# Performance work log

Measured on AMD Instinct MI355X. Metric: run time of the kernel, lower is better.

Reference implementation:

```python
import jax, jax.numpy as jnp
import numpy as np

VOCAB = 32000
DIM = 512
FFN = 4 * DIM
LAYERS_PER_BLOCK = [2, 2, 2]
THRESHOLDS = [3.5e-05, 4.0e-05, 1.0]
N_LAYERS = sum(LAYERS_PER_BLOCK)
B, S = 4, 1024


def setup_inputs() -> dict:
    key = jax.random.key(0)
    ks = jax.random.split(key, 8)
    x = jax.random.randint(ks[0], (B, S), 0, VOCAB)
    emb = jax.random.normal(ks[1], (VOCAB, DIM), jnp.float32) * 0.02
    head = jax.random.normal(ks[2], (VOCAB, DIM), jnp.float32) * (1.0 / np.sqrt(DIM))
    Wv = jax.random.normal(ks[3], (N_LAYERS, DIM, DIM), jnp.float32) * 0.02
    Wo = jax.random.normal(ks[4], (N_LAYERS, DIM, DIM), jnp.float32) * 0.02
    W1 = jax.random.normal(ks[5], (N_LAYERS, DIM, FFN), jnp.float32) * 0.02
    W2 = jax.random.normal(ks[6], (N_LAYERS, FFN, DIM), jnp.float32) * 0.02
    ln1_s = jnp.ones((N_LAYERS, DIM), jnp.float32)
    ln1_b = jnp.zeros((N_LAYERS, DIM), jnp.float32)
    ln2_s = jnp.ones((N_LAYERS, DIM), jnp.float32)
    ln2_b = jnp.zeros((N_LAYERS, DIM), jnp.float32)
    return {"x": x, "emb": emb, "head": head, "Wv": Wv, "Wo": Wo,
            "W1": W1, "W2": W2, "ln1_s": ln1_s, "ln1_b": ln1_b,
            "ln2_s": ln2_s, "ln2_b": ln2_b}


def _ln(x, s, b):
    m = jnp.mean(x, axis=-1, keepdims=True)
    v = jnp.mean((x - m) ** 2, axis=-1, keepdims=True)
    return (x - m) * jax.lax.rsqrt(v + 1e-5) * s + b


def reference(x, emb, head, Wv, Wo, W1, W2, ln1_s, ln1_b, ln2_s, ln2_b):
    T = B * S
    h = emb[x.reshape(-1)]                      # (T, dim) embedding gather
    active = jnp.ones((T,), dtype=bool)
    final_logits = jnp.zeros((T, VOCAB), jnp.float32)
    layer = 0
    n_blocks = len(LAYERS_PER_BLOCK)
    for b_idx, (n_l, thr) in enumerate(zip(LAYERS_PER_BLOCK, THRESHOLDS)):
        hb = h
        for l in range(layer, layer + n_l):
            # seq_len==1 attention: softmax over single key == 1 -> out = V @ Wo
            hn = _ln(hb, ln1_s[l], ln1_b[l])
            hb = hb + (hn @ Wv[l]) @ Wo[l]
            hn2 = _ln(hb, ln2_s[l], ln2_b[l])
            hb = hb + jax.nn.gelu(hn2 @ W1[l]) @ W2[l]
        layer += n_l
        logits = hb @ head.T                    # (T, vocab)
        conf = jnp.max(jax.nn.softmax(logits, axis=-1), axis=-1)
        is_last = b_idx == n_blocks - 1
        should_exit = conf > thr
        exit_now = active & (should_exit | is_last)   # scatter exiting tokens
        final_logits = jnp.where(exit_now[:, None], logits, final_logits)
        cont = active & ~exit_now
        h = jnp.where(cont[:, None], hb, h)           # only continuing tokens updated
        active = cont
    return final_logits.reshape(B, S, VOCAB)
```

## Files before the change

### kernel.cpp

```cpp
#include <hip/hip_runtime.h>
#include <hip/hip_bf16.h>
#include <math.h>

#define TT 4096
#define DIM 512
#define FFN 2048
#define NVOCAB 32000

typedef __attribute__((ext_vector_type(8))) short short8_t;
typedef __attribute__((ext_vector_type(4))) float f32x4;

__device__ __forceinline__ float gelu_f(float x) {
    float x3 = x * x * x;
    float u = 0.7978845608028654f * (x + 0.044715f * x3);
    return 0.5f * x * (1.0f + tanhf(u));
}

__device__ __forceinline__ unsigned short f2bf_rn(float f) {
    unsigned u = __float_as_uint(f);
    u += 0x7FFFu + ((u >> 16) & 1u);
    return (unsigned short)(u >> 16);
}

__global__ __launch_bounds__(128) void gather_kernel(const int* __restrict__ x,
                                                     const float* __restrict__ emb,
                                                     float* __restrict__ h,
                                                     int* __restrict__ flags) {
    int t = blockIdx.x;
    int idx = x[t];
    const float4 v = *(const float4*)&emb[(size_t)idx * DIM + threadIdx.x * 4];
    *(float4*)&h[(size_t)t * DIM + threadIdx.x * 4] = v;
    if (threadIdx.x == 0) flags[t] = 1;
}

__global__ __launch_bounds__(256) void cvt_hilo(const float* __restrict__ src,
                                                short* __restrict__ hi,
                                                short* __restrict__ lo, int n4) {
    int i = blockIdx.x * 256 + threadIdx.x;
    if (i >= n4) return;
    float4 v = *(const float4*)&src[(size_t)i * 4];
    float f[4] = {v.x, v.y, v.z, v.w};
    short4 hv, lv;
    short* hp = &hv.x;
    short* lp = &lv.x;
#pragma unroll
    for (int j = 0; j < 4; ++j) {
        unsigned short hb = f2bf_rn(f[j]);
        float hf = __uint_as_float((unsigned)hb << 16);
        unsigned short lb = f2bf_rn(f[j] - hf);
        hp[j] = (short)hb;
        lp[j] = (short)lb;
    }
    *(short4*)&hi[(size_t)i * 4] = hv;
    *(short4*)&lo[(size_t)i * 4] = lv;
}

__global__ __launch_bounds__(256) void cvt_bf16(const float* __restrict__ src,
                                                short* __restrict__ hi, int n4) {
    int i = blockIdx.x * 256 + threadIdx.x;
    if (i >= n4) return;
    float4 v = *(const float4*)&src[(size_t)i * 4];
    float f[4] = {v.x, v.y, v.z, v.w};
    short4 hv;
    short* hp = &hv.x;
#pragma unroll
    for (int j = 0; j < 4; ++j) hp[j] = (short)f2bf_rn(f[j]);
    *(short4*)&hi[(size_t)i * 4] = hv;
}

__global__ __launch_bounds__(256) void cvt_w_t(const float* __restrict__ W,
                                               short* __restrict__ hiT,
                                               short* __restrict__ loT,
                                               int K, int N) {
    __shared__ short hs[32][36];
    __shared__ short ls[32][36];
    const int n0 = blockIdx.x * 32, k0 = blockIdx.y * 32;
    const int r = threadIdx.x >> 3, c4 = (threadIdx.x & 7) << 2;
    float4 v = *(const float4*)&W[(size_t)(k0 + r) * N + n0 + c4];
    float f[4] = {v.x, v.y, v.z, v.w};
#pragma unroll
    for (int j = 0; j < 4; ++j) {
        unsigned short hb = f2bf_rn(f[j]);
        float hf = __uint_as_float((unsigned)hb << 16);
        unsigned short lb = f2bf_rn(f[j] - hf);
        hs[r][c4 + j] = (short)hb;
        ls[r][c4 + j] = (short)lb;
    }
    __syncthreads();
    const int nr = threadIdx.x >> 3, kc4 = (threadIdx.x & 7) << 2;
    short4 hv, lv;
    short* hp = &hv.x;
    short* lp = &lv.x;
#pragma unroll
    for (int j = 0; j < 4; ++j) {
        hp[j] = hs[kc4 + j][nr];
        lp[j] = ls[kc4 + j][nr];
    }
    *(short4*)&hiT[(size_t)(n0 + nr) * K + k0 + kc4] = hv;
    *(short4*)&loT[(size_t)(n0 + nr) * K + k0 + kc4] = lv;
}

template<bool IDX>
__global__ __launch_bounds__(256) void ln_kernel(const float* __restrict__ x,
                                                 const float* __restrict__ gam,
                                                 const float* __restrict__ bet,
                                                 float* __restrict__ out,
                                                 const int* __restrict__ idx,
                                                 const int* __restrict__ cnt) {
    int wv = threadIdx.x >> 6, lane = threadIdx.x & 63;
    int p = (blockIdx.x << 2) | wv;
    if (IDX && p >= *cnt) return;
    int t = IDX ? idx[p] : p;
    const float* row = x + (size_t)t * DIM;
    int base = lane * 8;
    float4 v0 = *(const float4*)&row[base];
    float4 v1 = *(const float4*)&row[base + 4];
    float s = v0.x + v0.y + v0.z + v0.w + v1.x + v1.y + v1.z + v1.w;
#pragma unroll
    for (int o = 32; o; o >>= 1) s += __shfl_xor(s, o, 64);
    float mean = s * (1.0f / (float)DIM);
    float d0 = v0.x - mean, d1 = v0.y - mean, d2 = v0.z - mean, d3 = v0.w - mean;
    float d4 = v1.x - mean, d5 = v1.y - mean, d6 = v1.z - mean, d7 = v1.w - mean;
    float q = d0*d0 + d1*d1 + d2*d2 + d3*d3 + d4*d4 + d5*d5 + d6*d6 + d7*d7;
#pragma unroll
    for (int o = 32; o; o >>= 1) q += __shfl_xor(q, o, 64);
    float var = q * (1.0f / (float)DIM);
    float rs = 1.0f / sqrtf(var + 1e-5f);
    float4 g0 = *(const float4*)&gam[base];
    float4 g1 = *(const float4*)&gam[base + 4];
    float4 b0 = *(const float4*)&bet[base];
    float4 b1 = *(const float4*)&bet[base + 4];
    float4 o0, o1;
    o0.x = d0 * rs * g0.x + b0.x;  o0.y = d1 * rs * g0.y + b0.y;
    o0.z = d2 * rs * g0.z + b0.z;  o0.w = d3 * rs * g0.w + b0.w;
    o1.x = d4 * rs * g1.x + b1.x;  o1.y = d5 * rs * g1.y + b1.y;
    o1.z = d6 * rs * g1.z + b1.z;  o1.w = d7 * rs * g1.w + b1.w;
    float* orow = out + (size_t)p * DIM;
    *(float4*)&orow[base] = o0;
    *(float4*)&orow[base + 4] = o1;
}

__global__ __launch_bounds__(256) void ln_hilo(const float* __restrict__ x,
                                               const float* __restrict__ gam,
                                               const float* __restrict__ bet,
                                               short* __restrict__ ohi,
                                               short* __restrict__ olo) {
    int wv = threadIdx.x >> 6, lane = threadIdx.x & 63;
    int t = (blockIdx.x << 2) | wv;
    const float* row = x + (size_t)t * DIM;
    int base = lane * 8;
    float4 v0 = *(const float4*)&row[base];
    float4 v1 = *(const float4*)&row[base + 4];
    float s = v0.x + v0.y + v0.z + v0.w + v1.x + v1.y + v1.z + v1.w;
#pragma unroll
    for (int o = 32; o; o >>= 1) s += __shfl_xor(s, o, 64);
    float mean = s * (1.0f / (float)DIM);
    float d[8] = {v0.x - mean, v0.y - mean, v0.z - mean, v0.w - mean,
                  v1.x - mean, v1.y - mean, v1.z - mean, v1.w - mean};
    float q = 0.0f;
#pragma unroll
    for (int j = 0; j < 8; ++j) q += d[j] * d[j];
#pragma unroll
    for (int o = 32; o; o >>= 1) q += __shfl_xor(q, o, 64);
    float var = q * (1.0f / (float)DIM);
    float rs = 1.0f / sqrtf(var + 1e-5f);
    float g[8], bb[8];
    *(float4*)&g[0] = *(const float4*)&gam[base];
    *(float4*)&g[4] = *(const float4*)&gam[base + 4];
    *(float4*)&bb[0] = *(const float4*)&bet[base];
    *(float4*)&bb[4] = *(const float4*)&bet[base + 4];
    short8_t hv, lv;
#pragma unroll
    for (int j = 0; j < 8; ++j) {
        float val = d[j] * rs * g[j] + bb[j];
        unsigned short hb = f2bf_rn(val);
        float hf = __uint_as_float((unsigned)hb << 16);
        hv[j] = (short)hb;
        lv[j] = (short)f2bf_rn(val - hf);
    }
    *(short8_t*)&ohi[(size_t)t * DIM + base] = hv;
    *(short8_t*)&olo[(size_t)t * DIM + base] = lv;
}

template<int EPI>
__global__ __launch_bounds__(256) void gemm_l_mfma(const short* __restrict__ Ah,
                                                   const short* __restrict__ Al,
                                                   const short* __restrict__ Bh,
                                                   const short* __restrict__ Bl,
                                                   float* __restrict__ Cf,
                                                   short* __restrict__ oHi,
                                                   short* __restrict__ oLo,
                                                   int N, int K) {
    __shared__ __align__(16) short sm[16384];
    short* sAh = sm;
    short* sAl = sm + 4096;
    short* sBh = sm + 8192;
    short* sBl = sm + 12288;
    const int tid = threadIdx.x;
    const int wv = tid >> 6, lane = tid & 63;
    const int m0 = blockIdx.x * 128;
    const int n0 = blockIdx.y * 128;
    const int wm = (wv & 1) * 64, wn = (wv >> 1) * 64;
    const int r16 = lane >> 2;
    const int gsw = ((lane & 3) ^ (r16 & 3)) << 3;
    const int fr = lane & 15;
    const int q = lane >> 4;

    f32x4 acc[4][4];
#pragma unroll
    for (int i = 0; i < 4; ++i)
#pragma unroll
        for (int j = 0; j < 4; ++j)
            acc[i][j] = (f32x4){0.0f, 0.0f, 0.0f, 0.0f};

    const int NKT = K >> 5;
    for (int kt = 0; kt < NKT; ++kt) {
        const int k0 = kt << 5;
        __syncthreads();
#pragma unroll
        for (int j = 0; j < 2; ++j) {
            const int rr = (wv << 5) + (j << 4);
            const int gr = rr + r16;
            const short* ga_h = Ah + (size_t)(m0 + gr) * K + k0 + gsw;
            const short* ga_l = Al + (size_t)(m0 + gr) * K + k0 + gsw;
            const short* gb_h = Bh + (size_t)(n0 + gr) * K + k0 + gsw;
            const short* gb_l = Bl + (size_t)(n0 + gr) * K + k0 + gsw;
            __builtin_amdgcn_global_load_lds((const __attribute__((address_space(1))) void*)ga_h,
                                             (__attribute__((address_space(3))) void*)(sAh + rr * 32), 16, 0, 0);
            __builtin_amdgcn_global_load_lds((const __attribute__((address_space(1))) void*)ga_l,
                                             (__attribute__((address_space(3))) void*)(sAl + rr * 32), 16, 0, 0);
            __builtin_amdgcn_global_load_lds((const __attribute__((address_space(1))) void*)gb_h,
                                             (__attribute__((address_space(3))) void*)(sBh + rr * 32), 16, 0, 0);
            __builtin_amdgcn_global_load_lds((const __attribute__((address_space(1))) void*)gb_l,
                                             (__attribute__((address_space(3))) void*)(sBl + rr * 32), 16, 0, 0);
        }
        __syncthreads();
        short8_t ah[4], al[4], bh[4], bl[4];
#pragma unroll
        for (int i = 0; i < 4; ++i) {
            const int ra = wm + i * 16 + fr;
            const int rb = wn + i * 16 + fr;
            const int swa = (q ^ (fr & 3)) << 3;
            ah[i] = *(const short8_t*)&sAh[ra * 32 + swa];
            al[i] = *(const short8_t*)&sAl[ra * 32 + swa];
            bh[i] = *(const short8_t*)&sBh[rb * 32 + swa];
            bl[i] = *(const short8_t*)&sBl[rb * 32 + swa];
        }
#pragma unroll
        for (int i = 0; i < 4; ++i)
#pragma unroll
            for (int j = 0; j < 4; ++j) {
                acc[i][j] = __builtin_amdgcn_mfma_f32_16x16x32_bf16(ah[i], bh[j], acc[i][j], 0, 0, 0);
                acc[i][j] = __builtin_amdgcn_mfma_f32_16x16x32_bf16(ah[i], bl[j], acc[i][j], 0, 0, 0);
                acc[i][j] = __builtin_amdgcn_mfma_f32_16x16x32_bf16(al[i], bh[j], acc[i][j], 0, 0, 0);
            }
    }
    const int row_base = (lane >> 4) << 2;
#pragma unroll
    for (int i = 0; i < 4; ++i)
#pragma unroll
        for (int j = 0; j < 4; ++j) {
            const int row = m0 + wm + i * 16 + row_base;
            const int col = n0 + wn + j * 16 + fr;
#pragma unroll
            for (int r = 0; r < 4; ++r) {
                float val = acc[i][j][r];
                if (EPI == 3) {
                    Cf[(size_t)(row + r) * N + col] = val;
                } else if (EPI == 2) {
                    Cf[(size_t)(row + r) * N + col] += val;
                } else if (EPI == 4) {
                    float* cp = &Cf[(size_t)(row + r) * N + col];
                    float nv = *cp + val;
                    *cp = nv;
                    unsigned short hb = f2bf_rn(nv);
                    float hf = __uint_as_float((unsigned)hb << 16);
                    oHi[(size_t)(row + r) * N + col] = (short)hb;
                    oLo[(size_t)(row + r) * N + col] = (short)f2bf_rn(nv - hf);
                } else {
                    if (EPI == 1) val = gelu_f(val);
                    unsigned short hb = f2bf_rn(val);
                    float hf = __uint_as_float((unsigned)hb << 16);
                    oHi[(size_t)(row + r) * N + col] = (short)hb;
                    oLo[(size_t)(row + r) * N + col] = (short)f2bf_rn(val - hf);
                }
            }
        }
}

__global__ __launch_bounds__(256) void gemm_head_bf16(const short* __restrict__ Ah,
                                                      const short* __restrict__ Bh,
                                                      float* __restrict__ C,
                                                      int N, int K) {
    __shared__ __align__(16) short sm[8192];
    short* sA = sm;
    short* sB = sm + 4096;
    const int tid = threadIdx.x;
    const int wv = tid >> 6, lane = tid & 63;
    const int m0 = blockIdx.x * 128;
    const int n0 = blockIdx.y * 128;
    const int wm = (wv & 1) * 64, wn = (wv >> 1) * 64;
    const int r16 = lane >> 2;
    const int gsw = ((lane & 3) ^ (r16 & 3)) << 3;
    const int fr = lane & 15;
    const int q = lane >> 4;

    f32x4 acc[4][4];
#pragma unroll
    for (int i = 0; i < 4; ++i)
#pragma unroll
        for (int j = 0; j < 4; ++j)
            acc[i][j] = (f32x4){0.0f, 0.0f, 0.0f, 0.0f};

    const int NKT = K >> 5;
    for (int kt = 0; kt < NKT; ++kt) {
        const int k0 = kt << 5;
        __syncthreads();
#pragma unroll
        for (int j = 0; j < 2; ++j) {
            const int rr = (wv << 5) + (j << 4);
            const int gr = rr + r16;
            const short* ga = Ah + (size_t)(m0 + gr) * K + k0 + gsw;
            const short* gb = Bh + (size_t)(n0 + gr) * K + k0 + gsw;
            __builtin_amdgcn_global_load_lds((const __attribute__((address_space(1))) void*)ga,
                                             (__attribute__((address_space(3))) void*)(sA + rr * 32), 16, 0, 0);
            __builtin_amdgcn_global_load_lds((const __attribute__((address_space(1))) void*)gb,
                                             (__attribute__((address_space(3))) void*)(sB + rr * 32), 16, 0, 0);
        }
        __syncthreads();
        short8_t ah[4], bh[4];
        const int swa = (q ^ (fr & 3)) << 3;
#pragma unroll
        for (int i = 0; i < 4; ++i) {
            ah[i] = *(const short8_t*)&sA[(wm + i * 16 + fr) * 32 + swa];
            bh[i] = *(const short8_t*)&sB[(wn + i * 16 + fr) * 32 + swa];
        }
#pragma unroll
        for (int i = 0; i < 4; ++i)
#pragma unroll
            for (int j = 0; j < 4; ++j)
                acc[i][j] = __builtin_amdgcn_mfma_f32_16x16x32_bf16(ah[i], bh[j], acc[i][j], 0, 0, 0);
    }
    const int row_base = (lane >> 4) << 2;
#pragma unroll
    for (int i = 0; i < 4; ++i)
#pragma unroll
        for (int j = 0; j < 4; ++j) {
            const int row = m0 + wm + i * 16 + row_base;
            const int col = n0 + wn + j * 16 + fr;
#pragma unroll
            for (int r = 0; r < 4; ++r)
                C[(size_t)(row + r) * N + col] = acc[i][j][r];
        }
}

template<int EPI>
__global__ __launch_bounds__(256) void gemm_l64(const short* __restrict__ Ah,
                                                const short* __restrict__ Al,
                                                const short* __restrict__ Bh,
                                                const short* __restrict__ Bl,
                                                float* __restrict__ Cf,
                                                short* __restrict__ oHi,
                                                short* __restrict__ oLo,
                                                int N, int K) {
    __shared__ __align__(16) short sm[12288];
    short* sAh = sm;
    short* sAl = sm + 2048;
    short* sBh = sm + 4096;
    short* sBl = sm + 8192;
    const int tid = threadIdx.x;
    const int wv = tid >> 6, lane = tid & 63;
    const int m0 = blockIdx.x * 64;
    const int n0 = blockIdx.y * 128;
    const int wm = (wv & 1) * 32, wn = (wv >> 1) * 64;
    const int r16 = lane >> 2;
    const int gsw = ((lane & 3) ^ (r16 & 3)) << 3;
    const int fr = lane & 15;
    const int q = lane >> 4;

    f32x4 acc[2][4];
#pragma unroll
    for (int i = 0; i < 2; ++i)
#pragma unroll
        for (int j = 0; j < 4; ++j)
            acc[i][j] = (f32x4){0.0f, 0.0f, 0.0f, 0.0f};

    const int NKT = K >> 5;
    for (int kt = 0; kt < NKT; ++kt) {
        const int k0 = kt << 5;
        __syncthreads();
        {
            const int rr = wv << 4;
            const int gr = rr + r16;
            const short* ga_h = Ah + (size_t)(m0 + gr) * K + k0 + gsw;
            const short* ga_l = Al + (size_t)(m0 + gr) * K + k0 + gsw;
            __builtin_amdgcn_global_load_lds((const __attribute__((address_space(1))) void*)ga_h,
                                             (__attribute__((address_space(3))) void*)(sAh + rr * 32), 16, 0, 0);
            __builtin_amdgcn_global_load_lds((const __attribute__((address_space(1))) void*)ga_l,
                                             (__attribute__((address_space(3))) void*)(sAl + rr * 32), 16, 0, 0);
        }
#pragma unroll
        for (int j = 0; j < 2; ++j) {
            const int rr = (wv << 5) + (j << 4);
            const int gr = rr + r16;
            const short* gb_h = Bh + (size_t)(n0 + gr) * K + k0 + gsw;
            const short* gb_l = Bl + (size_t)(n0 + gr) * K + k0 + gsw;
            __builtin_amdgcn_global_load_lds((const __attribute__((address_space(1))) void*)gb_h,
                                             (__attribute__((address_space(3))) void*)(sBh + rr * 32), 16, 0, 0);
            __builtin_amdgcn_global_load_lds((const __attribute__((address_space(1))) void*)gb_l,
                                             (__attribute__((address_space(3))) void*)(sBl + rr * 32), 16, 0, 0);
        }
        __syncthreads();
        short8_t ah[2], al[2], bh[4], bl[4];
        const int swa = (q ^ (fr & 3)) << 3;
#pragma unroll
        for (int i = 0; i < 2; ++i) {
            const int ra = wm + i * 16 + fr;
            ah[i] = *(const short8_t*)&sAh[ra * 32 + swa];
            al[i] = *(const short8_t*)&sAl[ra * 32 + swa];
        }
#pragma unroll
        for (int j = 0; j < 4; ++j) {
            const int rb = wn + j * 16 + fr;
            bh[j] = *(const short8_t*)&sBh[rb * 32 + swa];
            bl[j] = *(const short8_t*)&sBl[rb * 32 + swa];
        }
#pragma unroll
        for (int i = 0; i < 2; ++i)
#pragma unroll
            for (int j = 0; j < 4; ++j) {
                acc[i][j] = __builtin_amdgcn_mfma_f32_16x16x32_bf16(ah[i], bh[j], acc[i][j], 0, 0, 0);
                acc[i][j] = __builtin_amdgcn_mfma_f32_16x16x32_bf16(ah[i], bl[j], acc[i][j], 0, 0, 0);
                acc[i][j] = __builtin_amdgcn_mfma_f32_16x16x32_bf16(al[i], bh[j], acc[i][j], 0, 0, 0);
            }
    }
    const int row_base = (lane >> 4) << 2;
#pragma unroll
    for (int i = 0; i < 2; ++i)
#pragma unroll
        for (int j = 0; j < 4; ++j) {
            const int row = m0 + wm + i * 16 + row_base;
            const int col = n0 + wn + j * 16 + fr;
#pragma unroll
            for (int r = 0; r < 4; ++r) {
                float val = acc[i][j][r];
                if (EPI == 3) {
                    Cf[(size_t)(row + r) * N + col] = val;
                } else if (EPI == 2) {
                    Cf[(size_t)(row + r) * N + col] += val;
                } else if (EPI == 4) {
                    float* cp = &Cf[(size_t)(row + r) * N + col];
                    float nv = *cp + val;
                    *cp = nv;
                    unsigned short hb = f2bf_rn(nv);
                    float hf = __uint_as_float((unsigned)hb << 16);
                    oHi[(size_t)(row + r) * N + col] = (short)hb;
                    oLo[(size_t)(row + r) * N + col] = (short)f2bf_rn(nv - hf);
                } else {
                    if (EPI == 1) val = gelu_f(val);
                    unsigned short hb = f2bf_rn(val);
                    float hf = __uint_as_float((unsigned)hb << 16);
                    oHi[(size_t)(row + r) * N + col] = (short)hb;
                    oLo[(size_t)(row + r) * N + col] = (short)f2bf_rn(val - hf);
                }
            }
        }
}

template<bool ADD, bool GELU>
__global__ __launch_bounds__(256) void gemm_nn(const float* __restrict__ A,
                                               const float* __restrict__ B,
                                               float* __restrict__ C,
                                               int M, int N, int K) {
    const int m0 = blockIdx.y * 64, n0 = blockIdx.x * 64;
    __shared__ float As[16][68];
    __shared__ float Bs[16][68];
    const int tid = threadIdx.x;
    const int am = tid >> 2, ak = (tid & 3) << 2;
    const int bk = tid >> 4, bn = (tid & 15) << 2;
    const int tn = tid & 15, tm = tid >> 4;
    float acc[4][4] = {};
    for (int k0 = 0; k0 < K; k0 += 16) {
        float4 a4 = *(const float4*)&A[(size_t)(m0 + am) * K + k0 + ak];
        float4 b4 = *(const float4*)&B[(size_t)(k0 + bk) * N + n0 + bn];
        __syncthreads();
        As[ak + 0][am] = a4.x;
        As[ak + 1][am] = a4.y;
        As[ak + 2][am] = a4.z;
        As[ak + 3][am] = a4.w;
        *(float4*)&Bs[bk][bn] = b4;
        __syncthreads();
#pragma unroll
        for (int kk = 0; kk < 16; ++kk) {
            float4 av = *(const float4*)&As[kk][tm << 2];
            float4 bv = *(const float4*)&Bs[kk][tn << 2];
            float a[4] = {av.x, av.y, av.z, av.w};
            float b[4] = {bv.x, bv.y, bv.z, bv.w};
#pragma unroll
            for (int i = 0; i < 4; ++i)
#pragma unroll
                for (int j = 0; j < 4; ++j)
                    acc[i][j] = fmaf(a[i], b[j], acc[i][j]);
        }
    }
#pragma unroll
    for (int i = 0; i < 4; ++i) {
        size_t row = (size_t)(m0 + (tm << 2) + i);
        float* cp = &C[row * (size_t)N + n0 + (tn << 2)];
        float rr[4] = {acc[i][0], acc[i][1], acc[i][2], acc[i][3]};
        if (GELU) {
#pragma unroll
            for (int j = 0; j < 4; ++j) rr[j] = gelu_f(rr[j]);
        }
        if (ADD) {
            float4 cc = *(const float4*)cp;
            rr[0] += cc.x; rr[1] += cc.y; rr[2] += cc.z; rr[3] += cc.w;
        }
        float4 rv = {rr[0], rr[1], rr[2], rr[3]};
        *(float4*)cp = rv;
    }
}

template<bool ADD, bool GELU, bool SCAT>
__global__ __launch_bounds__(256) void gemm_nn_gs(const float* __restrict__ A,
                                                  const float* __restrict__ B,
                                                  float* __restrict__ C,
                                                  int N, int K,
                                                  const int* __restrict__ idx,
                                                  const int* __restrict__ cnt) {
    const int c = *cnt;
    const int ntm = (c + 63) >> 6;
    const int ntn = N >> 6;
    const int total = ntm * ntn;
    __shared__ float As[16][68];
    __shared__ float Bs[16][68];
    const int tid = threadIdx.x;
    const int am = tid >> 2, ak = (tid & 3) << 2;
    const int bk = tid >> 4, bn = (tid & 15) << 2;
    const int tn = tid & 15, tm = tid >> 4;
    for (int tile = blockIdx.x; tile < total; tile += gridDim.x) {
        const int m0 = (tile % ntm) << 6, n0 = (tile / ntm) << 6;
        int ar = m0 + am;
        ar = ar < c ? ar : c - 1;
        float acc[4][4] = {};
        for (int k0 = 0; k0 < K; k0 += 16) {
            float4 a4 = *(const float4*)&A[(size_t)ar * K + k0 + ak];
            float4 b4 = *(const float4*)&B[(size_t)(k0 + bk) * N + n0 + bn];
            __syncthreads();
            As[ak + 0][am] = a4.x;
            As[ak + 1][am] = a4.y;
            As[ak + 2][am] = a4.z;
            As[ak + 3][am] = a4.w;
            *(float4*)&Bs[bk][bn] = b4;
            __syncthreads();
#pragma unroll
            for (int kk = 0; kk < 16; ++kk) {
                float4 av = *(const float4*)&As[kk][tm << 2];
                float4 bv = *(const float4*)&Bs[kk][tn << 2];
                float a[4] = {av.x, av.y, av.z, av.w};
                float b[4] = {bv.x, bv.y, bv.z, bv.w};
#pragma unroll
                for (int i = 0; i < 4; ++i)
#pragma unroll
                    for (int j = 0; j < 4; ++j)
                        acc[i][j] = fmaf(a[i], b[j], acc[i][j]);
            }
        }
#pragma unroll
        for (int i = 0; i < 4; ++i) {
            int p = m0 + (tm << 2) + i;
            if (p >= c) continue;
            int r = SCAT ? idx[p] : p;
            float* cp = &C[(size_t)r * N + n0 + (tn << 2)];
            float rr[4] = {acc[i][0], acc[i][1], acc[i][2], acc[i][3]};
            if (GELU) {
#pragma unroll
                for (int j = 0; j < 4; ++j) rr[j] = gelu_f(rr[j]);
            }
            if (ADD) {
                float4 cc = *(const float4*)cp;
                rr[0] += cc.x; rr[1] += cc.y; rr[2] += cc.z; rr[3] += cc.w;
            }
            float4 rv = {rr[0], rr[1], rr[2], rr[3]};
            *(float4*)cp = rv;
        }
        __syncthreads();
    }
}

__global__ __launch_bounds__(256) void gemm_nt_head_gs(const float* __restrict__ A,
                                                       const float* __restrict__ Bt,
                                                       float* __restrict__ C,
                                                       const int* __restrict__ idx,
                                                       const int* __restrict__ cnt) {
    const int c = *cnt;
    const int ntm = (c + 63) >> 6;
    const int ntn = NVOCAB >> 6;
    const int total = ntm * ntn;
    __shared__ float As[16][68];
    __shared__ float Bs[16][68];
    const int tid = threadIdx.x;
    const int am = tid >> 2, ak = (tid & 3) << 2;
    const int tn = tid & 15, tm = tid >> 4;
    for (int tile = blockIdx.x; tile < total; tile += gridDim.x) {
        const int m0 = (tile % ntm) << 6, n0 = (tile / ntm) << 6;
        int ap = m0 + am;
        int ar = idx[ap < c ? ap : c - 1];
        float acc[4][4] = {};
        for (int k0 = 0; k0 < DIM; k0 += 16) {
            float4 a4 = *(const float4*)&A[(size_t)ar * DIM + k0 + ak];
            float4 b4 = *(const float4*)&Bt[(size_t)(n0 + am) * DIM + k0 + ak];
            __syncthreads();
            As[ak + 0][am] = a4.x;
            As[ak + 1][am] = a4.y;
            As[ak + 2][am] = a4.z;
            As[ak + 3][am] = a4.w;
            Bs[ak + 0][am] = b4.x;
            Bs[ak + 1][am] = b4.y;
            Bs[ak + 2][am] = b4.z;
            Bs[ak + 3][am] = b4.w;
            __syncthreads();
#pragma unroll
            for (int kk = 0; kk < 16; ++kk) {
                float4 av = *(const float4*)&As[kk][tm << 2];
                float4 bv = *(const float4*)&Bs[kk][tn << 2];
                float a[4] = {av.x, av.y, av.z, av.w};
                float b[4] = {bv.x, bv.y, bv.z, bv.w};
#pragma unroll
                for (int i = 0; i < 4; ++i)
#pragma unroll
                    for (int j = 0; j < 4; ++j)
                        acc[i][j] = fmaf(a[i], b[j], acc[i][j]);
            }
        }
#pragma unroll
        for (int i = 0; i < 4; ++i) {
            int p = m0 + (tm << 2) + i;
            if (p >= c) continue;
            int r = idx[p];
            float4 rv = {acc[i][0], acc[i][1], acc[i][2], acc[i][3]};
            *(float4*)&C[(size_t)r * NVOCAB + n0 + (tn << 2)] = rv;
        }
        __syncthreads();
    }
}

template<bool IDX>
__global__ __launch_bounds__(256) void conf_exit(const float* __restrict__ out,
                                                 int* __restrict__ flags,
                                                 const int* __restrict__ idx,
                                                 const int* __restrict__ cnt,
                                                 float thr) {
    int t;
    if (IDX) {
        if (blockIdx.x >= *cnt) return;
        t = idx[blockIdx.x];
    } else {
        t = blockIdx.x;
        if (flags[t] == 0) return;
    }
    const float4* row = (const float4*)(out + (size_t)t * NVOCAB);
    float m = -INFINITY, s = 0.0f;
    for (int i = threadIdx.x; i < NVOCAB / 4; i += 256) {
        float4 v = row[i];
        float m4 = fmaxf(fmaxf(v.x, v.y), fmaxf(v.z, v.w));
        float s4 = __expf(v.x - m4) + __expf(v.y - m4) + __expf(v.z - m4) + __expf(v.w - m4);
        if (m4 > m) {
            s = s * __expf(m - m4) + s4;
            m = m4;
        } else {
            s += s4 * __expf(m4 - m);
        }
    }
    __shared__ float ms[256], ss[256];
    ms[threadIdx.x] = m;
    ss[threadIdx.x] = s;
    __syncthreads();
    for (int st = 128; st; st >>= 1) {
        if (threadIdx.x < st) {
            float m1 = ms[threadIdx.x], s1 = ss[threadIdx.x];
            float m2 = ms[threadIdx.x + st], s2 = ss[threadIdx.x + st];
            float mm = fmaxf(m1, m2);
            ss[threadIdx.x] = s1 * __expf(m1 - mm) + s2 * __expf(m2 - mm);
            ms[threadIdx.x] = mm;
        }
        __syncthreads();
    }
    if (threadIdx.x == 0) {
        float conf = 1.0f / ss[0];
        if (conf > thr) flags[t] = 0;
    }
}

__global__ __launch_bounds__(256) void compact_kernel(const int* __restrict__ flags,
                                                      int* __restrict__ idx,
                                                      int* __restrict__ cnt) {
    __shared__ int wsum[4];
    __shared__ int base;
    if (threadIdx.x == 0) base = 0;
    int lane = threadIdx.x & 63, wv = threadIdx.x >> 6;
    for (int chunk = 0; chunk < TT; chunk += 256) {
        __syncthreads();
        int t = chunk + threadIdx.x;
        int f = flags[t];
        unsigned long long b = __ballot(f != 0);
        if (lane == 0) wsum[wv] = __popcll(b);
        __syncthreads();
        int off = base;
        for (int w = 0; w < wv; ++w) off += wsum[w];
        off += __popcll(b & ((1ull << lane) - 1));
        if (f) idx[off] = t;
        __syncthreads();
        if (threadIdx.x == 0) base += wsum[0] + wsum[1] + wsum[2] + wsum[3];
    }
    __syncthreads();
    if (threadIdx.x == 0) *cnt = base;
}

extern "C" void kernel_launch(void* const* d_in, const int* in_sizes, int n_in,
                              void* d_out, int out_size, void* d_ws, size_t ws_size,
                              hipStream_t stream) {
    const int* x = (const int*)d_in[0];
    const float* emb = (const float*)d_in[1];
    const float* head = (const float*)d_in[2];
    const float* Wv = (const float*)d_in[3];
    const float* Wo = (const float*)d_in[4];
    const float* W1 = (const float*)d_in[5];
    const float* W2 = (const float*)d_in[6];
    const float* ln1s = (const float*)d_in[7];
    const float* ln1b = (const float*)d_in[8];
    const float* ln2s = (const float*)d_in[9];
    const float* ln2b = (const float*)d_in[10];
    float* out = (float*)d_out;
    float* ws = (float*)d_ws;

    float* h  = ws;
    float* hn = ws + 2097152;
    float* tA = ws + 4194304;
    float* tF = ws + 6291456;
    short* hnHi = (short*)hn;
    short* hnLo = hnHi + TT * DIM;
    short* tAHi = (short*)tA;
    short* tALo = tAHi + TT * DIM;
    short* tFHi = (short*)tF;
    short* tFLo = tFHi + TT * FFN;
    int* flags = (int*)(ws + 14680064);
    int* idxl  = flags + TT;
    int* cntp  = flags + 2 * TT;
    short* hHi    = (short*)(ws + 14700000);
    short* hLo    = (short*)(ws + 15748576);
    short* headHi = (short*)(ws + 16797152);
    short* headLo = (short*)(ws + 24989152);
    short* wT     = (short*)(ws + 33181152);
    const size_t LSTRIDE = 5242880;
    const size_t NEED_T2 = (size_t)33181152 * 4;
    const size_t NEED_T1 = (size_t)38424032 * 4;
    const int tier = ws_size >= NEED_T1 ? 1 : (ws_size >= NEED_T2 ? 2 : 3);

    gather_kernel<<<TT, 128, 0, stream>>>(x, emb, h, flags);

    const float THR[3] = {3.5e-05f, 4.0e-05f, 1.0f};
    const dim3 gDD(DIM / 64, TT / 64), gDF(FFN / 64, TT / 64), gHead(NVOCAB / 64, TT / 64);

    if (tier == 1) {
        for (int l = 0; l < 2; ++l) {
            short* wb = wT + (size_t)l * LSTRIDE;
            cvt_hilo<<<(DIM * DIM / 4 + 255) / 256, 256, 0, stream>>>(Wv + (size_t)l * DIM * DIM, tAHi, tALo, DIM * DIM / 4);
            cvt_w_t<<<dim3(DIM / 32, DIM / 32), 256, 0, stream>>>(Wo + (size_t)l * DIM * DIM, wb + 524288, wb + 786432, DIM, DIM);
            gemm_l64<0><<<dim3(DIM / 64, DIM / 128), 256, 0, stream>>>(
                wb + 524288, wb + 786432, tAHi, tALo, nullptr, wb, wb + 262144, DIM, DIM);
            cvt_w_t<<<dim3(FFN / 32, DIM / 32), 256, 0, stream>>>(W1 + (size_t)l * DIM * FFN, wb + 1048576, wb + 2097152, DIM, FFN);
            cvt_w_t<<<dim3(DIM / 32, FFN / 32), 256, 0, stream>>>(W2 + (size_t)l * FFN * DIM, wb + 3145728, wb + 4194304, FFN, DIM);
        }
        for (int l = 0; l < 2; ++l) {
            short* wb = wT + (size_t)l * LSTRIDE;
            ln_hilo<<<TT / 4, 256, 0, stream>>>(h, ln1s + l * DIM, ln1b + l * DIM, hnHi, hnLo);
            gemm_l64<2><<<dim3(TT / 64, DIM / 128), 256, 0, stream>>>(hnHi, hnLo, wb, wb + 262144, h, nullptr, nullptr, DIM, DIM);
            ln_hilo<<<TT / 4, 256, 0, stream>>>(h, ln2s + l * DIM, ln2b + l * DIM, hnHi, hnLo);
            gemm_l_mfma<1><<<dim3(TT / 128, FFN / 128), 256, 0, stream>>>(hnHi, hnLo, wb + 1048576, wb + 2097152, nullptr, tFHi, tFLo, FFN, DIM);
            if (l == 1) {
                gemm_l64<4><<<dim3(TT / 64, DIM / 128), 256, 0, stream>>>(tFHi, tFLo, wb + 3145728, wb + 4194304, h, hHi, hLo, DIM, FFN);
            } else {
                gemm_l64<2><<<dim3(TT / 64, DIM / 128), 256, 0, stream>>>(tFHi, tFLo, wb + 3145728, wb + 4194304, h, nullptr, nullptr, DIM, FFN);
            }
        }
        cvt_bf16<<<(NVOCAB * DIM / 4 + 255) / 256, 256, 0, stream>>>(head, headHi, NVOCAB * DIM / 4);
        gemm_head_bf16<<<dim3(TT / 128, NVOCAB / 128), 256, 0, stream>>>(hHi, headHi, out, NVOCAB, DIM);
        conf_exit<false><<<TT, 256, 0, stream>>>(out, flags, nullptr, nullptr, THR[0]);
    } else {
        for (int l = 0; l < 2; ++l) {
            ln_kernel<false><<<TT / 4, 256, 0, stream>>>(h, ln1s + l * DIM, ln1b + l * DIM, hn, nullptr, nullptr);
            gemm_nn<false, false><<<gDD, 256, 0, stream>>>(hn, Wv + (size_t)l * DIM * DIM, tA, TT, DIM, DIM);
            gemm_nn<true, false><<<gDD, 256, 0, stream>>>(tA, Wo + (size_t)l * DIM * DIM, h, TT, DIM, DIM);
            ln_kernel<false><<<TT / 4, 256, 0, stream>>>(h, ln2s + l * DIM, ln2b + l * DIM, hn, nullptr, nullptr);
            gemm_nn<false, true><<<gDF, 256, 0, stream>>>(hn, W1 + (size_t)l * DIM * FFN, tF, TT, FFN, DIM);
            gemm_nn<true, false><<<gDD, 256, 0, stream>>>(tF, W2 + (size_t)l * FFN * DIM, h, TT, DIM, FFN);
        }
        if (tier == 2) {
            cvt_hilo<<<(TT * DIM / 4 + 255) / 256, 256, 0, stream>>>(h, hHi, hLo, TT * DIM / 4);
            cvt_hilo<<<(NVOCAB * DIM / 4 + 255) / 256, 256, 0, stream>>>(head, headHi, headLo, NVOCAB * DIM / 4);
            gemm_l_mfma<3><<<dim3(TT / 128, NVOCAB / 128), 256, 0, stream>>>(hHi, hLo, headHi, headLo, out, nullptr, nullptr, NVOCAB, DIM);
        } else {
            compact_kernel<<<1, 256, 0, stream>>>(flags, idxl, cntp);
            gemm_nt_head_gs<<<2048, 256, 0, stream>>>(h, head, out, idxl, cntp);
        }
        conf_exit<false><<<TT, 256, 0, stream>>>(out, flags, nullptr, nullptr, THR[0]);
    }
    compact_kernel<<<1, 256, 0, stream>>>(flags, idxl, cntp);

    for (int b = 1; b < 3; ++b) {
        for (int li = 0; li < 2; ++li) {
            int l = b * 2 + li;
            ln_kernel<true><<<TT / 4, 256, 0, stream>>>(h, ln1s + l * DIM, ln1b + l * DIM, hn, idxl, cntp);
            gemm_nn_gs<false, false, false><<<1024, 256, 0, stream>>>(hn, Wv + (size_t)l * DIM * DIM, tA, DIM, DIM, idxl, cntp);
            gemm_nn_gs<true, false, true><<<1024, 256, 0, stream>>>(tA, Wo + (size_t)l * DIM * DIM, h, DIM, DIM, idxl, cntp);
            ln_kernel<true><<<TT / 4, 256, 0, stream>>>(h, ln2s + l * DIM, ln2b + l * DIM, hn, idxl, cntp);
            gemm_nn_gs<false, true, false><<<1024, 256, 0, stream>>>(hn, W1 + (size_t)l * DIM * FFN, tF, FFN, DIM, idxl, cntp);
            gemm_nn_gs<true, false, true><<<1024, 256, 0, stream>>>(tF, W2 + (size_t)l * FFN * DIM, h, DIM, FFN, idxl, cntp);
        }
        gemm_nt_head_gs<<<2048, 256, 0, stream>>>(h, head, out, idxl, cntp);
        if (b == 1) {
            conf_exit<true><<<TT, 256, 0, stream>>>(out, flags, idxl, cntp, THR[1]);
            compact_kernel<<<1, 256, 0, stream>>>(flags, idxl, cntp);
        }
    }
}
```

Baseline: 794.0 us.

## Drop weight-lo split term in block-0 GEMMs and shrink gather-GEMM grids

Adds gemm_l2 and gemm_l64b kernels that multiply split hi/lo activations against only the bf16-hi weights. This cuts the three-MFMA split product to two and stops loading the weight-lo tiles in the block-0 layer GEMMs. Separately, the launch grids of the compacted gather GEMMs drop from 1024/2048 blocks to 256/512 blocks, which reduces idle blocks when few tokens remain active. Leaving out the weight-lo term lowers accuracy and could shift which tokens pass the early-exit thresholds.

```diff
diff --git a/kernel.cpp b/kernel.cpp
--- a/kernel.cpp
+++ b/kernel.cpp
@@ -180,6 +180,28 @@
     }
     *(short8_t*)&ohi[(size_t)t * DIM + base] = hv;
     *(short8_t*)&olo[(size_t)t * DIM + base] = lv;
+}
+
+__device__ __forceinline__ void epi_store(int EPI, float val, size_t off,
+                                          float* Cf, short* oHi, short* oLo) {
+    if (EPI == 3) {
+        Cf[off] = val;
+    } else if (EPI == 2) {
+        Cf[off] += val;
+    } else if (EPI == 4) {
+        float nv = Cf[off] + val;
+        Cf[off] = nv;
+        unsigned short hb = f2bf_rn(nv);
+        float hf = __uint_as_float((unsigned)hb << 16);
+        oHi[off] = (short)hb;
+        oLo[off] = (short)f2bf_rn(nv - hf);
+    } else {
+        if (EPI == 1) val = gelu_f(val);
+        unsigned short hb = f2bf_rn(val);
+        float hf = __uint_as_float((unsigned)hb << 16);
+        oHi[off] = (short)hb;
+        oLo[off] = (short)f2bf_rn(val - hf);
+    }
 }
 
 template<int EPI>
@@ -263,38 +285,23 @@
             const int row = m0 + wm + i * 16 + row_base;
             const int col = n0 + wn + j * 16 + fr;
 #pragma unroll
-            for (int r = 0; r < 4; ++r) {
-                float val = acc[i][j][r];
-                if (EPI == 3) {
-                    Cf[(size_t)(row + r) * N + col] = val;
-                } else if (EPI == 2) {
-                    Cf[(size_t)(row + r) * N + col] += val;
-                } else if (EPI == 4) {
-                    float* cp = &Cf[(size_t)(row + r) * N + col];
-                    float nv = *cp + val;
-                    *cp = nv;
-                    unsigned short hb = f2bf_rn(nv);
-                    float hf = __uint_as_float((unsigned)hb << 16);
-                    oHi[(size_t)(row + r) * N + col] = (short)hb;
-                    oLo[(size_t)(row + r) * N + col] = (short)f2bf_rn(nv - hf);
-                } else {
-                    if (EPI == 1) val = gelu_f(val);
-                    unsigned short hb = f2bf_rn(val);
-                    float hf = __uint_as_float((unsigned)hb << 16);
-                    oHi[(size_t)(row + r) * N + col] = (short)hb;
-                    oLo[(size_t)(row + r) * N + col] = (short)f2bf_rn(val - hf);
-                }
-            }
-        }
-}
-
-__global__ __launch_bounds__(256) void gemm_head_bf16(const short* __restrict__ Ah,
-                                                      const short* __restrict__ Bh,
-                                                      float* __restrict__ C,
-                                                      int N, int K) {
-    __shared__ __align__(16) short sm[8192];
-    short* sA = sm;
-    short* sB = sm + 4096;
+            for (int r = 0; r < 4; ++r)
+                epi_store(EPI, acc[i][j][r], (size_t)(row + r) * N + col, Cf, oHi, oLo);
+        }
+}
+
+template<int EPI>
+__global__ __launch_bounds__(256) void gemm_l2(const short* __restrict__ Ah,
+                                               const short* __restrict__ Al,
+                                               const short* __restrict__ Bh,
+                                               float* __restrict__ Cf,
+                                               short* __restrict__ oHi,
+                                               short* __restrict__ oLo,
+                                               int N, int K) {
+    __shared__ __align__(16) short sm[12288];
+    short* sAh = sm;
+    short* sAl = sm + 4096;
+    short* sBh = sm + 8192;
     const int tid = threadIdx.x;
     const int wv = tid >> 6, lane = tid & 63;
     const int m0 = blockIdx.x * 128;
@@ -320,26 +327,34 @@
         for (int j = 0; j < 2; ++j) {
             const int rr = (wv << 5) + (j << 4);
             const int gr = rr + r16;
-            const short* ga = Ah + (size_t)(m0 + gr) * K + k0 + gsw;
-            const short* gb = Bh + (size_t)(n0 + gr) * K + k0 + gsw;
-            __builtin_amdgcn_global_load_lds((const __attribute__((address_space(1))) void*)ga,
-                                             (__attribute__((address_space(3))) void*)(sA + rr * 32), 16, 0, 0);
-            __builtin_amdgcn_global_load_lds((const __attribute__((address_space(1))) void*)gb,
-                                             (__attribute__((address_space(3))) void*)(sB + rr * 32), 16, 0, 0);
-        }
-        __syncthreads();
-        short8_t ah[4], bh[4];
-        const int swa = (q ^ (fr & 3)) << 3;
+            const short* ga_h = Ah + (size_t)(m0 + gr) * K + k0 + gsw;
+            const short* ga_l = Al + (size_t)(m0 + gr) * K + k0 + gsw;
+            const short* gb_h = Bh + (size_t)(n0 + gr) * K + k0 + gsw;
+            __builtin_amdgcn_global_load_lds((const __attribute__((address_space(1))) void*)ga_h,
+                                             (__attribute__((address_space(3))) void*)(sAh + rr * 32), 16, 0, 0);
+            __builtin_amdgcn_global_load_lds((const __attribute__((address_space(1))) void*)ga_l,
+                                             (__attribute__((address_space(3))) void*)(sAl + rr * 32), 16, 0, 0);
+            __builtin_amdgcn_global_load_lds((const __attribute__((address_space(1))) void*)gb_h,
+                                             (__attribute__((address_space(3))) void*)(sBh + rr * 32), 16, 0, 0);
+        }
+        __syncthreads();
+        short8_t ah[4], al[4], bh[4];
 #pragma unroll
         for (int i = 0; i < 4; ++i) {
-            ah[i] = *(const short8_t*)&sA[(wm + i * 16 + fr) * 32 + swa];
-            bh[i] = *(const short8_t*)&sB[(wn + i * 16 + fr) * 32 + swa];
+            const int ra = wm + i * 16 + fr;
+            const int rb = wn + i * 16 + fr;
+            const int swa = (q ^ (fr & 3)) << 3;
+            ah[i] = *(const short8_t*)&sAh[ra * 32 + swa];
+            al[i] = *(const short8_t*)&sAl[ra * 32 + swa];
+            bh[i] = *(const short8_t*)&sBh[rb * 32 + swa];
         }
 #pragma unroll
         for (int i = 0; i < 4; ++i)
 #pragma unroll
-            for (int j = 0; j < 4; ++j)
+            for (int j = 0; j < 4; ++j) {
                 acc[i][j] = __builtin_amdgcn_mfma_f32_16x16x32_bf16(ah[i], bh[j], acc[i][j], 0, 0, 0);
+                acc[i][j] = __builtin_amdgcn_mfma_f32_16x16x32_bf16(al[i], bh[j], acc[i][j], 0, 0, 0);
+            }
     }
     const int row_base = (lane >> 4) << 2;
 #pragma unroll
@@ -350,7 +365,93 @@
             const int col = n0 + wn + j * 16 + fr;
 #pragma unroll
             for (int r = 0; r < 4; ++r)
-                C[(size_t)(row + r) * N + col] = acc[i][j][r];
+                epi_store(EPI, acc[i][j][r], (size_t)(row + r) * N + col, Cf, oHi, oLo);
+        }
+}
+
+template<int EPI>
+__global__ __launch_bounds__(256) void gemm_l64b(const short* __restrict__ Ah,
+                                                 const short* __restrict__ Al,
+                                                 const short* __restrict__ Bh,
+                                                 float* __restrict__ Cf,
+                                                 short* __restrict__ oHi,
+                                                 short* __restrict__ oLo,
+                                                 int N, int K) {
+    __shared__ __align__(16) short sm[8192];
+    short* sAh = sm;
+    short* sAl = sm + 2048;
+    short* sBh = sm + 4096;
+    const int tid = threadIdx.x;
+    const int wv = tid >> 6, lane = tid & 63;
+    const int m0 = blockIdx.x * 64;
+    const int n0 = blockIdx.y * 128;
+    const int wm = (wv & 1) * 32, wn = (wv >> 1) * 64;
+    const int r16 = lane >> 2;
+    const int gsw = ((lane & 3) ^ (r16 & 3)) << 3;
+    const int fr = lane & 15;
+    const int q = lane >> 4;
+
+    f32x4 acc[2][4];
+#pragma unroll
+    for (int i = 0; i < 2; ++i)
+#pragma unroll
+        for (int j = 0; j < 4; ++j)
+            acc[i][j] = (f32x4){0.0f, 0.0f, 0.0f, 0.0f};
+
+    const int NKT = K >> 5;
+    for (int kt = 0; kt < NKT; ++kt) {
+        const int k0 = kt << 5;
+        __syncthreads();
+        {
+            const int rr = wv << 4;
+            const int gr = rr + r16;
+            const short* ga_h = Ah + (size_t)(m0 + gr) * K + k0 + gsw;
+            const short* ga_l = Al + (size_t)(m0 + gr) * K + k0 + gsw;
+            __builtin_amdgcn_global_load_lds((const __attribute__((address_space(1))) void*)ga_h,
+                                             (__attribute__((address_space(3))) void*)(sAh + rr * 32), 16, 0, 0);
+            __builtin_amdgcn_global_load_lds((const __attribute__((address_space(1))) void*)ga_l,
+                                             (__attribute__((address_space(3))) void*)(sAl + rr * 32), 16, 0, 0);
+        }
+#pragma unroll
+        for (int j = 0; j < 2; ++j) {
+            const int rr = (wv << 5) + (j << 4);
+            const int gr = rr + r16;
+            const short* gb_h = Bh + (size_t)(n0 + gr) * K + k0 + gsw;
+            __builtin_amdgcn_global_load_lds((const __attribute__((address_space(1))) void*)gb_h,
+                                             (__attribute__((address_space(3))) void*)(sBh + rr * 32), 16, 0, 0);
+        }
+        __syncthreads();
+        short8_t ah[2], al[2], bh[4];
+        const int swa = (q ^ (fr & 3)) << 3;
+#pragma unroll
+        for (int i = 0; i < 2; ++i) {
+            const int ra = wm + i * 16 + fr;
+            ah[i] = *(const short8_t*)&sAh[ra * 32 + swa];
+            al[i] = *(const short8_t*)&sAl[ra * 32 + swa];
+        }
+#pragma unroll
+        for (int j = 0; j < 4; ++j) {
+            const int rb = wn + j * 16 + fr;
+            bh[j] = *(const short8_t*)&sBh[rb * 32 + swa];
+        }
+#pragma unroll
+        for (int i = 0; i < 2; ++i)
+#pragma unroll
+            for (int j = 0; j < 4; ++j) {
+                acc[i][j] = __builtin_amdgcn_mfma_f32_16x16x32_bf16(ah[i], bh[j], acc[i][j], 0, 0, 0);
+                acc[i][j] = __builtin_amdgcn_mfma_f32_16x16x32_bf16(al[i], bh[j], acc[i][j], 0, 0, 0);
+            }
+    }
+    const int row_base = (lane >> 4) << 2;
+#pragma unroll
+    for (int i = 0; i < 2; ++i)
+#pragma unroll
+        for (int j = 0; j < 4; ++j) {
+            const int row = m0 + wm + i * 16 + row_base;
+            const int col = n0 + wn + j * 16 + fr;
+#pragma unroll
+            for (int r = 0; r < 4; ++r)
+                epi_store(EPI, acc[i][j][r], (size_t)(row + r) * N + col, Cf, oHi, oLo);
         }
 }
 
@@ -442,28 +543,74 @@
             const int row = m0 + wm + i * 16 + row_base;
             const int col = n0 + wn + j * 16 + fr;
 #pragma unroll
-            for (int r = 0; r < 4; ++r) {
-                float val = acc[i][j][r];
-                if (EPI == 3) {
-                    Cf[(size_t)(row + r) * N + col] = val;
-                } else if (EPI == 2) {
-                    Cf[(size_t)(row + r) * N + col] += val;
-                } else if (EPI == 4) {
-                    float* cp = &Cf[(size_t)(row + r) * N + col];
-                    float nv = *cp + val;
-                    *cp = nv;
-                    unsigned short hb = f2bf_rn(nv);
-                    float hf = __uint_as_float((unsigned)hb << 16);
-                    oHi[(size_t)(row + r) * N + col] = (short)hb;
-                    oLo[(size_t)(row + r) * N + col] = (short)f2bf_rn(nv - hf);
-                } else {
-                    if (EPI == 1) val = gelu_f(val);
-                    unsigned short hb = f2bf_rn(val);
-                    float hf = __uint_as_float((unsigned)hb << 16);
-                    oHi[(size_t)(row + r) * N + col] = (short)hb;
-                    oLo[(size_t)(row + r) * N + col] = (short)f2bf_rn(val - hf);
-                }
-            }
+            for (int r = 0; r < 4; ++r)
+                epi_store(EPI, acc[i][j][r], (size_t)(row + r) * N + col, Cf, oHi, oLo);
+        }
+}
+
+__global__ __launch_bounds__(256) void gemm_head_bf16(const short* __restrict__ Ah,
+                                                      const short* __restrict__ Bh,
+                                                      float* __restrict__ C,
+                                                      int N, int K) {
+    __shared__ __align__(16) short sm[8192];
+    short* sA = sm;
+    short* sB = sm + 4096;
+    const int tid = threadIdx.x;
+    const int wv = tid >> 6, lane = tid & 63;
+    const int m0 = blockIdx.x * 128;
+    const int n0 = blockIdx.y * 128;
+    const int wm = (wv & 1) * 64, wn = (wv >> 1) * 64;
+    const int r16 = lane >> 2;
+    const int gsw = ((lane & 3) ^ (r16 & 3)) << 3;
+    const int fr = lane & 15;
+    const int q = lane >> 4;
+
+    f32x4 acc[4][4];
+#pragma unroll
+    for (int i = 0; i < 4; ++i)
+#pragma unroll
+        for (int j = 0; j < 4; ++j)
+            acc[i][j] = (f32x4){0.0f, 0.0f, 0.0f, 0.0f};
+
+    const int NKT = K >> 5;
+    for (int kt = 0; kt < NKT; ++kt) {
+        const int k0 = kt << 5;
+        __syncthreads();
+#pragma unroll
+        for (int j = 0; j < 2; ++j) {
+            const int rr = (wv << 5) + (j << 4);
+            const int gr = rr + r16;
+            const short* ga = Ah + (size_t)(m0 + gr) * K + k0 + gsw;
+            const short* gb = Bh + (size_t)(n0 + gr) * K + k0 + gsw;
+            __builtin_amdgcn_global_load_lds((const __attribute__((address_space(1))) void*)ga,
+                                             (__attribute__((address_space(3))) void*)(sA + rr * 32), 16, 0, 0);
+            __builtin_amdgcn_global_load_lds((const __attribute__((address_space(1))) void*)gb,
+                                             (__attribute__((address_space(3))) void*)(sB + rr * 32), 16, 0, 0);
+        }
+        __syncthreads();
+        short8_t ah[4], bh[4];
+        const int swa = (q ^ (fr & 3)) << 3;
+#pragma unroll
+        for (int i = 0; i < 4; ++i) {
+            ah[i] = *(const short8_t*)&sA[(wm + i * 16 + fr) * 32 + swa];
+            bh[i] = *(const short8_t*)&sB[(wn + i * 16 + fr) * 32 + swa];
+        }
+#pragma unroll
+        for (int i = 0; i < 4; ++i)
+#pragma unroll
+            for (int j = 0; j < 4; ++j)
+                acc[i][j] = __builtin_amdgcn_mfma_f32_16x16x32_bf16(ah[i], bh[j], acc[i][j], 0, 0, 0);
+    }
+    const int row_base = (lane >> 4) << 2;
+#pragma unroll
+    for (int i = 0; i < 4; ++i)
+#pragma unroll
+        for (int j = 0; j < 4; ++j) {
+            const int row = m0 + wm + i * 16 + row_base;
+            const int col = n0 + wn + j * 16 + fr;
+#pragma unroll
+            for (int r = 0; r < 4; ++r)
+                C[(size_t)(row + r) * N + col] = acc[i][j][r];
         }
 }
 
@@ -775,13 +922,13 @@
         for (int l = 0; l < 2; ++l) {
             short* wb = wT + (size_t)l * LSTRIDE;
             ln_hilo<<<TT / 4, 256, 0, stream>>>(h, ln1s + l * DIM, ln1b + l * DIM, hnHi, hnLo);
-            gemm_l64<2><<<dim3(TT / 64, DIM / 128), 256, 0, stream>>>(hnHi, hnLo, wb, wb + 262144, h, nullptr, nullptr, DIM, DIM);
+            gemm_l64b<2><<<dim3(TT / 64, DIM / 128), 256, 0, stream>>>(hnHi, hnLo, wb, h, nullptr, nullptr, DIM, DIM);
             ln_hilo<<<TT / 4, 256, 0, stream>>>(h, ln2s + l * DIM, ln2b + l * DIM, hnHi, hnLo);
-            gemm_l_mfma<1><<<dim3(TT / 128, FFN / 128), 256, 0, stream>>>(hnHi, hnLo, wb + 1048576, wb + 2097152, nullptr, tFHi, tFLo, FFN, DIM);
+            gemm_l2<1><<<dim3(TT / 128, FFN / 128), 256, 0, stream>>>(hnHi, hnLo, wb + 1048576, nullptr, tFHi, tFLo, FFN, DIM);
             if (l == 1) {
-                gemm_l64<4><<<dim3(TT / 64, DIM / 128), 256, 0, stream>>>(tFHi, tFLo, wb + 3145728, wb + 4194304, h, hHi, hLo, DIM, FFN);
+                gemm_l64b<4><<<dim3(TT / 64, DIM / 128), 256, 0, stream>>>(tFHi, tFLo, wb + 3145728, h, hHi, hLo, DIM, FFN);
             } else {
-                gemm_l64<2><<<dim3(TT / 64, DIM / 128), 256, 0, stream>>>(tFHi, tFLo, wb + 3145728, wb + 4194304, h, nullptr, nullptr, DIM, FFN);
+                gemm_l64b<2><<<dim3(TT / 64, DIM / 128), 256, 0, stream>>>(tFHi, tFLo, wb + 3145728, h, nullptr, nullptr, DIM, FFN);
             }
         }
         cvt_bf16<<<(NVOCAB * DIM / 4 + 255) / 256, 256, 0, stream>>>(head, headHi, NVOCAB * DIM / 4);
@@ -802,7 +949,7 @@
             gemm_l_mfma<3><<<dim3(TT / 128, NVOCAB / 128), 256, 0, stream>>>(hHi, hLo, headHi, headLo, out, nullptr, nullptr, NVOCAB, DIM);
         } else {
             compact_kernel<<<1, 256, 0, stream>>>(flags, idxl, cntp);
-            gemm_nt_head_gs<<<2048, 256, 0, stream>>>(h, head, out, idxl, cntp);
+            gemm_nt_head_gs<<<512, 256, 0, stream>>>(h, head, out, idxl, cntp);
         }
         conf_exit<false><<<TT, 256, 0, stream>>>(out, flags, nullptr, nullptr, THR[0]);
     }
@@ -812,13 +959,13 @@
         for (int li = 0; li < 2; ++li) {
             int l = b * 2 + li;
             ln_kernel<true><<<TT / 4, 256, 0, stream>>>(h, ln1s + l * DIM, ln1b + l * DIM, hn, idxl, cntp);
-            gemm_nn_gs<false, false, false><<<1024, 256, 0, stream>>>(hn, Wv + (size_t)l * DIM * DIM, tA, DIM, DIM, idxl, cntp);
-            gemm_nn_gs<true, false, true><<<1024, 256, 0, stream>>>(tA, Wo + (size_t)l * DIM * DIM, h, DIM, DIM, idxl, cntp);
+            gemm_nn_gs<false, false, false><<<256, 256, 0, stream>>>(hn, Wv + (size_t)l * DIM * DIM, tA, DIM, DIM, idxl, cntp);
+            gemm_nn_gs<true, false, true><<<256, 256, 0, stream>>>(tA, Wo + (size_t)l * DIM * DIM, h, DIM, DIM, idxl, cntp);
             ln_kernel<true><<<TT / 4, 256, 0, stream>>>(h, ln2s + l * DIM, ln2b + l * DIM, hn, idxl, cntp);
-            gemm_nn_gs<false, true, false><<<1024, 256, 0, stream>>>(hn, W1 + (size_t)l * DIM * FFN, tF, FFN, DIM, idxl, cntp);
-            gemm_nn_gs<true, false, true><<<1024, 256, 0, stream>>>(tF, W2 + (size_t)l * FFN * DIM, h, DIM, FFN, idxl, cntp);
-        }
-        gemm_nt_head_gs<<<2048, 256, 0, stream>>>(h, head, out, idxl, cntp);
+            gemm_nn_gs<false, true, false><<<256, 256, 0, stream>>>(hn, W1 + (size_t)l * DIM * FFN, tF, FFN, DIM, idxl, cntp);
+            gemm_nn_gs<true, false, true><<<256, 256, 0, stream>>>(tF, W2 + (size_t)l * FFN * DIM, h, DIM, FFN, idxl, cntp);
+        }
+        gemm_nt_head_gs<<<512, 256, 0, stream>>>(h, head, out, idxl, cntp);
         if (b == 1) {
             conf_exit<true><<<TT, 256, 0, stream>>>(out, flags, idxl, cntp, THR[1]);
             compact_kernel<<<1, 256, 0, stream>>>(flags, idxl, cntp);
```

Result: faster. 742.1 us (-6.5%).
